# Kernel optimization log

Hardware: AMD Instinct MI355X
Metric: run time of the kernel (lower is better)

The kernel has to match this reference:

```python
import jax, jax.numpy as jnp
import numpy as np

NOISE_EPS = 1e-2


def setup_inputs() -> dict:
    key = jax.random.key(0)
    ks = jax.random.split(key, 6)
    N, D, E, H = 16384, 512, 8, 1024
    x = jax.random.normal(ks[0], (N, D), jnp.float32)
    eps = jax.random.normal(ks[1], (N, E), jnp.float32)
    w_gate = jax.random.normal(ks[2], (D, E), jnp.float32) * 0.02
    w_noise = jax.random.normal(ks[3], (D, E), jnp.float32) * 0.02
    W_h = jnp.eye(E, dtype=jnp.float32)  # module initializes W_h = eye(num_experts)
    W1 = jax.random.normal(ks[4], (E, D, H), jnp.float32) * 0.02
    b1 = jnp.zeros((E, H), jnp.float32)
    W2 = jax.random.normal(ks[5], (E, H, D), jnp.float32) * 0.02
    b2 = jnp.zeros((E, D), jnp.float32)
    return dict(x=x, eps=eps, w_gate=w_gate, w_noise=w_noise, W_h=W_h,
                W1=W1, b1=b1, W2=W2, b2=b2, k=2, capacity=5120)


def reference(x, eps, w_gate, w_noise, W_h, W1, b1, W2, b2, k, capacity):
    N, D = x.shape
    E = w_gate.shape[1]
    # --- noisy top-k gating ---
    clean_logits = (x @ w_gate) @ W_h                       # [N, E]
    noise_stddev = jax.nn.softplus(x @ w_noise) + NOISE_EPS  # [N, E]
    noisy_logits = clean_logits + eps * noise_stddev
    top_vals, top_idx = jax.lax.top_k(noisy_logits, k)       # [N, k]
    top_gates = jax.nn.softmax(top_vals, axis=-1)
    gates = jnp.zeros((N, E), x.dtype).at[jnp.arange(N)[:, None], top_idx].set(top_gates)
    # --- capacity masking: keep the first `capacity` routed tokens per expert (batch order) ---
    active = gates > 0
    rank = jnp.cumsum(active, axis=0) - 1                    # per-expert arrival rank
    keep = active & (rank < capacity)
    gates = jnp.where(keep, gates, jnp.zeros((), x.dtype))
    # --- dispatch into fixed [E, capacity] buffers (dummy slot absorbs dropped writes) ---
    flat = jnp.where(keep, jnp.arange(E)[None, :] * capacity + rank, E * capacity)  # [N, E]
    tok = jnp.broadcast_to(jnp.arange(N, dtype=jnp.int32)[:, None], (N, E))
    buf = jnp.zeros(E * capacity + 1, jnp.int32).at[flat].set(tok)[:E * capacity].reshape(E, capacity)
    gbuf = jnp.zeros(E * capacity + 1, x.dtype).at[flat].set(gates)[:E * capacity].reshape(E, capacity)
    x_exp = x[buf]                                           # [E, C, D] gather
    # --- per-expert 1-layer FFN (grouped GEMM) ---
    h = jax.nn.relu(jnp.einsum('ecd,edh->ech', x_exp, W1) + b1[:, None, :])
    y_exp = jnp.einsum('ech,eho->eco', h, W2) + b2[:, None, :]
    # --- weighted scatter-combine (unfilled slots have gate 0, so they add nothing) ---
    weighted = y_exp * gbuf[..., None]
    combined = jnp.zeros((N, D), x.dtype).at[buf.reshape(-1)].add(weighted.reshape(-1, D))
    return combined
```

## Files before the change

kernel.cpp:

```cpp
#include <hip/hip_runtime.h>
#include <hip/hip_bf16.h>
#include <cstdint>

#define NTOK 16384
#define DIM 512
#define NEXP 8
#define HID 1024
#define CAPACITY 5120

typedef __attribute__((ext_vector_type(8))) short bf16x8;
typedef __attribute__((ext_vector_type(4))) float f32x4;
typedef unsigned long long u64;

__device__ __forceinline__ unsigned short f2bf(float f) {
    unsigned u = __float_as_uint(f);
    unsigned r = (u + 0x7FFFu + ((u >> 16) & 1u)) >> 16;
    return (unsigned short)r;
}

#define GLDS16(gp, lp) __builtin_amdgcn_global_load_lds( \
    (const __attribute__((address_space(1))) void*)(gp), \
    (__attribute__((address_space(3))) void*)(lp), 16, 0, 0)

__global__ __launch_bounds__(256) void gating_kernel(
    const float* __restrict__ x, const float* __restrict__ eps,
    const float* __restrict__ wg, const float* __restrict__ wn,
    const float* __restrict__ Wh, int2* __restrict__ rec)
{
    int w = threadIdx.x >> 6, lane = threadIdx.x & 63;
    int n = blockIdx.x * 4 + w;
    float ag[8], an[8];
#pragma unroll
    for (int e = 0; e < 8; ++e) { ag[e] = 0.f; an[e] = 0.f; }
    const float* xr = x + (size_t)n * DIM;
#pragma unroll
    for (int i = 0; i < DIM / 64; ++i) {
        int d = i * 64 + lane;
        float xv = xr[d];
        const float4* g4 = reinterpret_cast<const float4*>(wg + (size_t)d * 8);
        const float4* n4 = reinterpret_cast<const float4*>(wn + (size_t)d * 8);
        float4 a0 = g4[0], a1 = g4[1], b0 = n4[0], b1v = n4[1];
        ag[0] += xv * a0.x; ag[1] += xv * a0.y; ag[2] += xv * a0.z; ag[3] += xv * a0.w;
        ag[4] += xv * a1.x; ag[5] += xv * a1.y; ag[6] += xv * a1.z; ag[7] += xv * a1.w;
        an[0] += xv * b0.x; an[1] += xv * b0.y; an[2] += xv * b0.z; an[3] += xv * b0.w;
        an[4] += xv * b1v.x; an[5] += xv * b1v.y; an[6] += xv * b1v.z; an[7] += xv * b1v.w;
    }
#pragma unroll
    for (int off = 32; off; off >>= 1) {
#pragma unroll
        for (int e = 0; e < 8; ++e) {
            ag[e] += __shfl_xor(ag[e], off);
            an[e] += __shfl_xor(an[e], off);
        }
    }
    float noisy[8];
#pragma unroll
    for (int e = 0; e < 8; ++e) {
        float c = 0.f;
#pragma unroll
        for (int j = 0; j < 8; ++j) c += ag[j] * Wh[j * 8 + e];
        float v = an[e];
        float sp = fmaxf(v, 0.f) + log1pf(expf(-fabsf(v)));
        noisy[e] = c + eps[(size_t)n * 8 + e] * (sp + 1e-2f);
    }
    int i1 = 0; float v1 = noisy[0];
#pragma unroll
    for (int e = 1; e < 8; ++e) if (noisy[e] > v1) { v1 = noisy[e]; i1 = e; }
    int i2 = -1; float v2 = -3.4e38f;
#pragma unroll
    for (int e = 0; e < 8; ++e) if (e != i1 && noisy[e] > v2) { v2 = noisy[e]; i2 = e; }
    float ex = expf(v2 - v1);
    float g1 = 1.f / (1.f + ex);
    if (lane == 0)
        rec[n] = make_int2(i1 | (i2 << 8), __float_as_int(g1));
}

__global__ __launch_bounds__(1024) void scan_local(
    const int2* __restrict__ rec, unsigned* __restrict__ lrank, int* __restrict__ btot)
{
    __shared__ u64 wtot[16];
    __shared__ int wprefix[16][8];
    int tid = threadIdx.x, w = tid >> 6, lane = tid & 63;
    int n = blockIdx.x * 1024 + tid;
    int2 r = rec[n];
    int e1 = r.x & 0xFF, e2 = (r.x >> 8) & 0xFF;
    u64 m = (1ULL << (e1 * 8)) | (1ULL << (e2 * 8));
    u64 incl = m;
#pragma unroll
    for (int off = 1; off < 64; off <<= 1) {
        u64 v = __shfl_up(incl, off);
        if (lane >= off) incl += v;
    }
    if (lane == 63) wtot[w] = incl;
    __syncthreads();
    if (tid < 128) {
        int e = tid & 7, ww = tid >> 3;
        int s = 0;
        for (int j = 0; j < ww; ++j) s += (int)((wtot[j] >> (e * 8)) & 0xFF);
        wprefix[ww][e] = s;
        if (ww == 15)
            btot[blockIdx.x * 8 + e] = s + (int)((wtot[15] >> (e * 8)) & 0xFF);
    }
    __syncthreads();
    u64 excl = incl - m;
    unsigned l1 = (unsigned)(wprefix[w][e1] + (int)((excl >> (e1 * 8)) & 0xFF));
    unsigned l2 = (unsigned)(wprefix[w][e2] + (int)((excl >> (e2 * 8)) & 0xFF));
    lrank[n] = l1 | (l2 << 16);
}

__global__ __launch_bounds__(64) void scan_offs(
    const int* __restrict__ btot, int* __restrict__ off, int* __restrict__ counts,
    const int* __restrict__ cap_p)
{
    int e = threadIdx.x;
    if (e >= 8) return;
    int cap = *cap_p; if (cap > CAPACITY) cap = CAPACITY;
    int run = 0;
    for (int b = 0; b < 16; ++b) {
        off[b * 8 + e] = run;
        run += btot[b * 8 + e];
    }
    counts[e] = min(run, cap);
}

__global__ __launch_bounds__(1024) void scatter_k(
    const int2* __restrict__ rec, const unsigned* __restrict__ lrank,
    const int* __restrict__ off, const int* __restrict__ cap_p,
    int* __restrict__ buf, float* __restrict__ gbuf)
{
    int tid = threadIdx.x, b = blockIdx.x;
    int n = b * 1024 + tid;
    int cap = *cap_p; if (cap > CAPACITY) cap = CAPACITY;
    int2 r = rec[n];
    int e1 = r.x & 0xFF, e2 = (r.x >> 8) & 0xFF;
    float g1 = __int_as_float(r.y), g2 = 1.f - g1;
    unsigned lr = lrank[n];
    int r1 = off[b * 8 + e1] + (int)(lr & 0xFFFF);
    int r2 = off[b * 8 + e2] + (int)(lr >> 16);
    if (r1 < cap) { buf[e1 * CAPACITY + r1] = n; gbuf[e1 * CAPACITY + r1] = g1; }
    if (r2 < cap) { buf[e2 * CAPACITY + r2] = n; gbuf[e2 * CAPACITY + r2] = g2; }
}

__global__ __launch_bounds__(256) void cvt_x(const float* __restrict__ in,
                                             unsigned short* __restrict__ out, int n)
{
    int i = (blockIdx.x * 256 + threadIdx.x) * 8;
    if (i >= n) return;
    float4 a = *reinterpret_cast<const float4*>(in + i);
    float4 b = *reinterpret_cast<const float4*>(in + i + 4);
    int4 v;
    v.x = f2bf(a.x) | ((int)f2bf(a.y) << 16);
    v.y = f2bf(a.z) | ((int)f2bf(a.w) << 16);
    v.z = f2bf(b.x) | ((int)f2bf(b.y) << 16);
    v.w = f2bf(b.z) | ((int)f2bf(b.w) << 16);
    *reinterpret_cast<int4*>(out + i) = v;
}

__global__ __launch_bounds__(256) void tcvt(const float* __restrict__ in,
                                            unsigned short* __restrict__ out, int R, int C)
{
    __shared__ float tile[32][33];
    int z = blockIdx.z;
    int c0 = blockIdx.x * 32, r0 = blockIdx.y * 32;
    int tx = threadIdx.x, ty = threadIdx.y;
    const float* inz = in + (size_t)z * R * C;
    unsigned short* outz = out + (size_t)z * R * C;
#pragma unroll
    for (int j = 0; j < 32; j += 8)
        tile[ty + j][tx] = inz[(size_t)(r0 + ty + j) * C + c0 + tx];
    __syncthreads();
#pragma unroll
    for (int j = 0; j < 32; j += 8)
        outz[(size_t)(c0 + ty + j) * R + r0 + tx] = f2bf(tile[tx][ty + j]);
}

template <int MODE>
__global__ __launch_bounds__(256, 4) void ffn_gemm(
    const unsigned short* __restrict__ A, const unsigned short* __restrict__ Bt,
    const float* __restrict__ bias, unsigned short* __restrict__ Hout,
    float* __restrict__ Out, const int* __restrict__ buf,
    const float* __restrict__ gbuf, const int* __restrict__ counts,
    int Ka, int Nd)
{
    int flat = blockIdx.x + gridDim.x * (blockIdx.y + gridDim.y * blockIdx.z);
    int e  = flat & 7;
    int rr = flat >> 3;
    int tn = rr % gridDim.y;
    int tmb = rr / gridDim.y;

    int cnt = counts[e];
    if (tmb * 256 >= cnt) return;
    int tid = threadIdx.x, w = tid >> 6, lane = tid & 63;
    int q = lane >> 4, rl = lane & 15;
    int ebase = e * CAPACITY;
    int wm = w >> 1, wn = w & 1;

    __shared__ __align__(16) char lds[32768];
    char* As = lds;
    char* Bs = lds + 16384;

    unsigned boff[4];
    int srow[4], skp[4];
#pragma unroll
    for (int i = 0; i < 4; ++i) {
        int p = (w * 4 + i) * 64 + lane;
        int row = p >> 3, kp = p & 7;
        int c = kp ^ (row & 7);
        srow[i] = row; skp[i] = c;
        boff[i] = (unsigned)(e * Nd + tn * 128 + row) * Ka + c * 8;
    }

    for (int it = 0; it < 2; ++it) {
        int tm = tmb * 2 + it;
        if (tm * 128 >= cnt) break;

        unsigned aoff[4];
#pragma unroll
        for (int i = 0; i < 4; ++i) {
            int slot = tm * 128 + srow[i];
            if (MODE == 1) {
                int tok = (slot < cnt) ? buf[ebase + slot] : 0;
                aoff[i] = (unsigned)tok * Ka + skp[i] * 8;
            } else {
                aoff[i] = (unsigned)(ebase + slot) * Ka + skp[i] * 8;
            }
        }

        f32x4 acc[4][4];
#pragma unroll
        for (int mi = 0; mi < 4; ++mi)
#pragma unroll
            for (int ni = 0; ni < 4; ++ni)
                acc[mi][ni] = (f32x4){0.f, 0.f, 0.f, 0.f};

        for (int k0 = 0; k0 < Ka; k0 += 64) {
#pragma unroll
            for (int i = 0; i < 4; ++i) {
                GLDS16(A + aoff[i] + k0, As + (w * 4 + i) * 1024);
                GLDS16(Bt + boff[i] + k0, Bs + (w * 4 + i) * 1024);
            }
            __syncthreads();
#pragma unroll
            for (int kk = 0; kk < 2; ++kk) {
                bf16x8 af[4], bfr[4];
#pragma unroll
                for (int mi = 0; mi < 4; ++mi) {
                    int row = wm * 64 + mi * 16 + rl;
                    int cc = (kk * 4 + q) ^ (row & 7);
                    af[mi] = *reinterpret_cast<const bf16x8*>(As + row * 128 + cc * 16);
                }
#pragma unroll
                for (int ni = 0; ni < 4; ++ni) {
                    int row = wn * 64 + ni * 16 + rl;
                    int cc = (kk * 4 + q) ^ (row & 7);
                    bfr[ni] = *reinterpret_cast<const bf16x8*>(Bs + row * 128 + cc * 16);
                }
#pragma unroll
                for (int mi = 0; mi < 4; ++mi)
#pragma unroll
                    for (int ni = 0; ni < 4; ++ni)
                        acc[mi][ni] = __builtin_amdgcn_mfma_f32_16x16x32_bf16(
                            af[mi], bfr[ni], acc[mi][ni], 0, 0, 0);
            }
            __syncthreads();
        }

        if (MODE == 1) {
#pragma unroll
            for (int ni = 0; ni < 4; ++ni) {
                int gcol = tn * 128 + wn * 64 + ni * 16 + rl;
                float bv = bias[e * Nd + gcol];
#pragma unroll
                for (int mi = 0; mi < 4; ++mi) {
#pragma unroll
                    for (int r = 0; r < 4; ++r) {
                        int grow = tm * 128 + wm * 64 + mi * 16 + q * 4 + r;
                        float v = fmaxf(acc[mi][ni][r] + bv, 0.f);
                        Hout[(size_t)(ebase + grow) * HID + gcol] = f2bf(v);
                    }
                }
            }
        } else {
#pragma unroll
            for (int ni = 0; ni < 4; ++ni) {
                int gcol = tn * 128 + wn * 64 + ni * 16 + rl;
                float bv = bias[e * Nd + gcol];
#pragma unroll
                for (int mi = 0; mi < 4; ++mi) {
#pragma unroll
                    for (int r = 0; r < 4; ++r) {
                        int grow = tm * 128 + wm * 64 + mi * 16 + q * 4 + r;
                        if (grow < cnt) {
                            int tok = buf[ebase + grow];
                            float g = gbuf[ebase + grow];
                            float v = (acc[mi][ni][r] + bv) * g;
                            atomicAdd(Out + (size_t)tok * DIM + gcol, v);
                        }
                    }
                }
            }
        }
    }
}

extern "C" void kernel_launch(void* const* d_in, const int* in_sizes, int n_in,
                              void* d_out, int out_size, void* d_ws, size_t ws_size,
                              hipStream_t stream)
{
    const float* x   = (const float*)d_in[0];
    const float* eps = (const float*)d_in[1];
    const float* wg  = (const float*)d_in[2];
    const float* wn  = (const float*)d_in[3];
    const float* Wh  = (const float*)d_in[4];
    const float* W1  = (const float*)d_in[5];
    const float* b1  = (const float*)d_in[6];
    const float* W2  = (const float*)d_in[7];
    const float* b2  = (const float*)d_in[8];
    const int* capp  = (const int*)d_in[10];

    char* ws = (char*)d_ws;
    unsigned short* xg   = (unsigned short*)(ws);
    unsigned short* w1t  = (unsigned short*)(ws + 41943040);
    unsigned short* w2t  = (unsigned short*)(ws + 50331648);
    unsigned short* hK   = (unsigned short*)(ws + 58720256);
    int*      buf    = (int*)     (ws + 142606336);
    float*    gbuf   = (float*)   (ws + 142770176);
    int2*     rec    = (int2*)    (ws + 142934016);
    unsigned* lrank  = (unsigned*)(ws + 143065088);
    int*      btot   = (int*)     (ws + 143130624);
    int*      off    = (int*)     (ws + 143131136);
    int*      counts = (int*)     (ws + 143131648);

    float* out = (float*)d_out;
    hipMemsetAsync(out, 0, (size_t)out_size * sizeof(float), stream);

    gating_kernel<<<NTOK / 4, 256, 0, stream>>>(x, eps, wg, wn, Wh, rec);
    scan_local<<<16, 1024, 0, stream>>>(rec, lrank, btot);
    scan_offs<<<1, 64, 0, stream>>>(btot, off, counts, capp);
    scatter_k<<<16, 1024, 0, stream>>>(rec, lrank, off, capp, buf, gbuf);
    cvt_x<<<NTOK * DIM / 8 / 256, 256, 0, stream>>>(x, xg, NTOK * DIM);
    tcvt<<<dim3(HID / 32, DIM / 32, NEXP), dim3(32, 8), 0, stream>>>(W1, w1t, DIM, HID);
    tcvt<<<dim3(DIM / 32, HID / 32, NEXP), dim3(32, 8), 0, stream>>>(W2, w2t, HID, DIM);

    ffn_gemm<1><<<dim3(CAPACITY / 256, HID / 128, NEXP), 256, 0, stream>>>(
        xg, w1t, b1, hK, nullptr, buf, gbuf, counts, DIM, HID);
    ffn_gemm<0><<<dim3(CAPACITY / 256, DIM / 128, NEXP), 256, 0, stream>>>(
        hK, w2t, b2, nullptr, out, buf, gbuf, counts, HID, DIM);
}
```

Before: 221.3 us.

## Triple-buffer GEMM k-loop with async LDS loads and explicit vmcnt waits

Replaces the single-buffered 64-wide k-step loop in the expert FFN GEMM with a three-stage ring of 32-wide k tiles in LDS. Loads for tile t+2 are issued before computing on tile t, and partial s_waitcnt vmcnt counts are used so global-to-LDS traffic overlaps MFMA work. The LDS swizzle changes to match 64-byte rows. LDS use rises to 48KB and occupancy is lowered to 3 blocks per CU. The hand-written waitcnt/barrier sequencing is fragile and depends on the compiler not adding other outstanding vector memory ops.

```diff
diff --git a/kernel.cpp b/kernel.cpp
--- a/kernel.cpp
+++ b/kernel.cpp
@@ -174,8 +174,19 @@
         outz[(size_t)(c0 + ty + j) * R + r0 + tx] = f2bf(tile[tx][ty + j]);
 }
 
+
+#define STAGE32(T, BI)                                           \
+  {                                                              \
+    int k0_ = (T) * 32;                                          \
+    char* d_ = lds + (BI) * 16384 + w * 2048;                    \
+    GLDS16(A + aoff[0] + k0_, d_);                               \
+    GLDS16(A + aoff[1] + k0_, d_ + 1024);                        \
+    GLDS16(Bt + boff[0] + k0_, d_ + 8192);                       \
+    GLDS16(Bt + boff[1] + k0_, d_ + 9216);                       \
+  }
+
 template <int MODE>
-__global__ __launch_bounds__(256, 4) void ffn_gemm(
+__global__ __launch_bounds__(256, 3) void ffn_gemm(
     const unsigned short* __restrict__ A, const unsigned short* __restrict__ Bt,
     const float* __restrict__ bias, unsigned short* __restrict__ Hout,
     float* __restrict__ Out, const int* __restrict__ buf,
@@ -195,34 +206,37 @@
     int ebase = e * CAPACITY;
     int wm = w >> 1, wn = w & 1;
 
-    __shared__ __align__(16) char lds[32768];
-    char* As = lds;
-    char* Bs = lds + 16384;
-
-    unsigned boff[4];
-    int srow[4], skp[4];
-#pragma unroll
-    for (int i = 0; i < 4; ++i) {
-        int p = (w * 4 + i) * 64 + lane;
-        int row = p >> 3, kp = p & 7;
-        int c = kp ^ (row & 7);
-        srow[i] = row; skp[i] = c;
-        boff[i] = (unsigned)(e * Nd + tn * 128 + row) * Ka + c * 8;
-    }
+    __shared__ __align__(16) char lds[49152];
+
+    int srow[2], skc[2];
+#pragma unroll
+    for (int i = 0; i < 2; ++i) {
+        int p = (w * 2 + i) * 64 + lane;
+        int row = p >> 2, kp = p & 3;
+        srow[i] = row;
+        skc[i] = kp ^ ((row >> 1) & 3);
+    }
+    unsigned boff[2];
+#pragma unroll
+    for (int i = 0; i < 2; ++i)
+        boff[i] = (unsigned)(e * Nd + tn * 128 + srow[i]) * Ka + skc[i] * 8;
+
+    int ccb = (q ^ ((rl >> 1) & 3)) << 4;
+    int nt = Ka >> 5;
 
     for (int it = 0; it < 2; ++it) {
         int tm = tmb * 2 + it;
         if (tm * 128 >= cnt) break;
 
-        unsigned aoff[4];
-#pragma unroll
-        for (int i = 0; i < 4; ++i) {
+        unsigned aoff[2];
+#pragma unroll
+        for (int i = 0; i < 2; ++i) {
             int slot = tm * 128 + srow[i];
             if (MODE == 1) {
                 int tok = (slot < cnt) ? buf[ebase + slot] : 0;
-                aoff[i] = (unsigned)tok * Ka + skp[i] * 8;
+                aoff[i] = (unsigned)tok * Ka + skc[i] * 8;
             } else {
-                aoff[i] = (unsigned)(ebase + slot) * Ka + skp[i] * 8;
+                aoff[i] = (unsigned)(ebase + slot) * Ka + skc[i] * 8;
             }
         }
 
@@ -233,36 +247,44 @@
             for (int ni = 0; ni < 4; ++ni)
                 acc[mi][ni] = (f32x4){0.f, 0.f, 0.f, 0.f};
 
-        for (int k0 = 0; k0 < Ka; k0 += 64) {
-#pragma unroll
-            for (int i = 0; i < 4; ++i) {
-                GLDS16(A + aoff[i] + k0, As + (w * 4 + i) * 1024);
-                GLDS16(Bt + boff[i] + k0, Bs + (w * 4 + i) * 1024);
-            }
-            __syncthreads();
-#pragma unroll
-            for (int kk = 0; kk < 2; ++kk) {
-                bf16x8 af[4], bfr[4];
-#pragma unroll
-                for (int mi = 0; mi < 4; ++mi) {
-                    int row = wm * 64 + mi * 16 + rl;
-                    int cc = (kk * 4 + q) ^ (row & 7);
-                    af[mi] = *reinterpret_cast<const bf16x8*>(As + row * 128 + cc * 16);
-                }
-#pragma unroll
-                for (int ni = 0; ni < 4; ++ni) {
-                    int row = wn * 64 + ni * 16 + rl;
-                    int cc = (kk * 4 + q) ^ (row & 7);
-                    bfr[ni] = *reinterpret_cast<const bf16x8*>(Bs + row * 128 + cc * 16);
-                }
-#pragma unroll
-                for (int mi = 0; mi < 4; ++mi)
-#pragma unroll
-                    for (int ni = 0; ni < 4; ++ni)
-                        acc[mi][ni] = __builtin_amdgcn_mfma_f32_16x16x32_bf16(
-                            af[mi], bfr[ni], acc[mi][ni], 0, 0, 0);
-            }
-            __syncthreads();
+        STAGE32(0, 0);
+        STAGE32(1, 1);
+
+        int bcur = 0, bst = 2;
+        for (int t = 0; t < nt; ++t) {
+            if (t + 2 < nt) {
+                STAGE32(t + 2, bst);
+                bst = (bst == 2) ? 0 : bst + 1;
+                asm volatile("s_waitcnt vmcnt(8)" ::: "memory");
+            } else if (t + 2 == nt) {
+                asm volatile("s_waitcnt vmcnt(4)" ::: "memory");
+            } else {
+                asm volatile("s_waitcnt vmcnt(0)" ::: "memory");
+            }
+            asm volatile("s_barrier" ::: "memory");
+
+            const char* As = lds + bcur * 16384;
+            const char* Bs = As + 8192;
+            bf16x8 af[4], bfr[4];
+#pragma unroll
+            for (int mi = 0; mi < 4; ++mi) {
+                int row = wm * 64 + mi * 16 + rl;
+                af[mi] = *reinterpret_cast<const bf16x8*>(As + row * 64 + ccb);
+            }
+#pragma unroll
+            for (int ni = 0; ni < 4; ++ni) {
+                int row = wn * 64 + ni * 16 + rl;
+                bfr[ni] = *reinterpret_cast<const bf16x8*>(Bs + row * 64 + ccb);
+            }
+#pragma unroll
+            for (int mi = 0; mi < 4; ++mi)
+#pragma unroll
+                for (int ni = 0; ni < 4; ++ni)
+                    acc[mi][ni] = __builtin_amdgcn_mfma_f32_16x16x32_bf16(
+                        af[mi], bfr[ni], acc[mi][ni], 0, 0, 0);
+
+            asm volatile("s_barrier" ::: "memory");
+            bcur = (bcur == 2) ? 0 : bcur + 1;
         }
 
         if (MODE == 1) {
```

Result: no change. 223.9 us (+1.2%).

## Compute both 128-row M tiles together to reuse B tile across 256 rows

Applied to the files above, without the earlier changes.

The grouped FFN GEMM used to process two 128-row M tiles one after the other, reloading the B (weight) tile for each. It now loads both A tiles and one B tile per k-step into a larger 48KB LDS buffer and keeps two accumulator sets, so each B fragment feeds twice as many MFMAs. This halves B traffic and barriers per output. In exchange it doubles accumulator registers and drops launch bounds to 2 blocks per CU, which lowers occupancy, and it computes the second tile even when it lies beyond the expert's token count.

```diff
diff --git a/kernel.cpp b/kernel.cpp
--- a/kernel.cpp
+++ b/kernel.cpp
@@ -175,7 +175,7 @@
 }
 
 template <int MODE>
-__global__ __launch_bounds__(256, 4) void ffn_gemm(
+__global__ __launch_bounds__(256, 2) void ffn_gemm(
     const unsigned short* __restrict__ A, const unsigned short* __restrict__ Bt,
     const float* __restrict__ bias, unsigned short* __restrict__ Hout,
     float* __restrict__ Out, const int* __restrict__ buf,
@@ -195,107 +195,112 @@
     int ebase = e * CAPACITY;
     int wm = w >> 1, wn = w & 1;
 
-    __shared__ __align__(16) char lds[32768];
-    char* As = lds;
-    char* Bs = lds + 16384;
-
-    unsigned boff[4];
-    int srow[4], skp[4];
+    __shared__ __align__(16) char lds[49152];
+
+    unsigned a0off[4], a1off[4], boff[4];
 #pragma unroll
     for (int i = 0; i < 4; ++i) {
         int p = (w * 4 + i) * 64 + lane;
         int row = p >> 3, kp = p & 7;
         int c = kp ^ (row & 7);
-        srow[i] = row; skp[i] = c;
+        int s0 = tmb * 256 + row, s1 = s0 + 128;
+        if (MODE == 1) {
+            int t0 = (s0 < cnt) ? buf[ebase + s0] : 0;
+            int t1 = (s1 < cnt) ? buf[ebase + s1] : 0;
+            a0off[i] = (unsigned)t0 * Ka + c * 8;
+            a1off[i] = (unsigned)t1 * Ka + c * 8;
+        } else {
+            a0off[i] = (unsigned)(ebase + s0) * Ka + c * 8;
+            a1off[i] = (unsigned)(ebase + s1) * Ka + c * 8;
+        }
         boff[i] = (unsigned)(e * Nd + tn * 128 + row) * Ka + c * 8;
     }
 
-    for (int it = 0; it < 2; ++it) {
-        int tm = tmb * 2 + it;
-        if (tm * 128 >= cnt) break;
-
-        unsigned aoff[4];
+    f32x4 acc0[4][4], acc1[4][4];
+#pragma unroll
+    for (int mi = 0; mi < 4; ++mi)
+#pragma unroll
+        for (int ni = 0; ni < 4; ++ni) {
+            acc0[mi][ni] = (f32x4){0.f, 0.f, 0.f, 0.f};
+            acc1[mi][ni] = (f32x4){0.f, 0.f, 0.f, 0.f};
+        }
+
+    for (int k0 = 0; k0 < Ka; k0 += 64) {
 #pragma unroll
         for (int i = 0; i < 4; ++i) {
-            int slot = tm * 128 + srow[i];
-            if (MODE == 1) {
-                int tok = (slot < cnt) ? buf[ebase + slot] : 0;
-                aoff[i] = (unsigned)tok * Ka + skp[i] * 8;
-            } else {
-                aoff[i] = (unsigned)(ebase + slot) * Ka + skp[i] * 8;
+            GLDS16(A + a0off[i] + k0, lds + (w * 4 + i) * 1024);
+            GLDS16(A + a1off[i] + k0, lds + 16384 + (w * 4 + i) * 1024);
+            GLDS16(Bt + boff[i] + k0, lds + 32768 + (w * 4 + i) * 1024);
+        }
+        __syncthreads();
+#pragma unroll
+        for (int kk = 0; kk < 2; ++kk) {
+            bf16x8 af0[4], af1[4], bfr[4];
+#pragma unroll
+            for (int mi = 0; mi < 4; ++mi) {
+                int row = wm * 64 + mi * 16 + rl;
+                int cc = (kk * 4 + q) ^ (row & 7);
+                af0[mi] = *reinterpret_cast<const bf16x8*>(lds + row * 128 + cc * 16);
+                af1[mi] = *reinterpret_cast<const bf16x8*>(lds + 16384 + row * 128 + cc * 16);
             }
-        }
-
-        f32x4 acc[4][4];
-#pragma unroll
-        for (int mi = 0; mi < 4; ++mi)
-#pragma unroll
-            for (int ni = 0; ni < 4; ++ni)
-                acc[mi][ni] = (f32x4){0.f, 0.f, 0.f, 0.f};
-
-        for (int k0 = 0; k0 < Ka; k0 += 64) {
-#pragma unroll
-            for (int i = 0; i < 4; ++i) {
-                GLDS16(A + aoff[i] + k0, As + (w * 4 + i) * 1024);
-                GLDS16(Bt + boff[i] + k0, Bs + (w * 4 + i) * 1024);
+#pragma unroll
+            for (int ni = 0; ni < 4; ++ni) {
+                int row = wn * 64 + ni * 16 + rl;
+                int cc = (kk * 4 + q) ^ (row & 7);
+                bfr[ni] = *reinterpret_cast<const bf16x8*>(lds + 32768 + row * 128 + cc * 16);
             }
-            __syncthreads();
-#pragma unroll
-            for (int kk = 0; kk < 2; ++kk) {
-                bf16x8 af[4], bfr[4];
-#pragma unroll
-                for (int mi = 0; mi < 4; ++mi) {
-                    int row = wm * 64 + mi * 16 + rl;
-                    int cc = (kk * 4 + q) ^ (row & 7);
-                    af[mi] = *reinterpret_cast<const bf16x8*>(As + row * 128 + cc * 16);
+#pragma unroll
+            for (int mi = 0; mi < 4; ++mi)
+#pragma unroll
+                for (int ni = 0; ni < 4; ++ni) {
+                    acc0[mi][ni] = __builtin_amdgcn_mfma_f32_16x16x32_bf16(
+                        af0[mi], bfr[ni], acc0[mi][ni], 0, 0, 0);
+                    acc1[mi][ni] = __builtin_amdgcn_mfma_f32_16x16x32_bf16(
+                        af1[mi], bfr[ni], acc1[mi][ni], 0, 0, 0);
                 }
-#pragma unroll
-                for (int ni = 0; ni < 4; ++ni) {
-                    int row = wn * 64 + ni * 16 + rl;
-                    int cc = (kk * 4 + q) ^ (row & 7);
-                    bfr[ni] = *reinterpret_cast<const bf16x8*>(Bs + row * 128 + cc * 16);
-                }
-#pragma unroll
-                for (int mi = 0; mi < 4; ++mi)
-#pragma unroll
-                    for (int ni = 0; ni < 4; ++ni)
-                        acc[mi][ni] = __builtin_amdgcn_mfma_f32_16x16x32_bf16(
-                            af[mi], bfr[ni], acc[mi][ni], 0, 0, 0);
-            }
-            __syncthreads();
-        }
-
-        if (MODE == 1) {
-#pragma unroll
-            for (int ni = 0; ni < 4; ++ni) {
-                int gcol = tn * 128 + wn * 64 + ni * 16 + rl;
-                float bv = bias[e * Nd + gcol];
-#pragma unroll
-                for (int mi = 0; mi < 4; ++mi) {
-#pragma unroll
-                    for (int r = 0; r < 4; ++r) {
-                        int grow = tm * 128 + wm * 64 + mi * 16 + q * 4 + r;
-                        float v = fmaxf(acc[mi][ni][r] + bv, 0.f);
-                        Hout[(size_t)(ebase + grow) * HID + gcol] = f2bf(v);
-                    }
+        }
+        __syncthreads();
+    }
+
+    if (MODE == 1) {
+#pragma unroll
+        for (int ni = 0; ni < 4; ++ni) {
+            int gcol = tn * 128 + wn * 64 + ni * 16 + rl;
+            float bv = bias[e * Nd + gcol];
+#pragma unroll
+            for (int mi = 0; mi < 4; ++mi) {
+#pragma unroll
+                for (int r = 0; r < 4; ++r) {
+                    int g0 = tmb * 256 + wm * 64 + mi * 16 + q * 4 + r;
+                    float v0 = fmaxf(acc0[mi][ni][r] + bv, 0.f);
+                    Hout[(size_t)(ebase + g0) * HID + gcol] = f2bf(v0);
+                    float v1 = fmaxf(acc1[mi][ni][r] + bv, 0.f);
+                    Hout[(size_t)(ebase + g0 + 128) * HID + gcol] = f2bf(v1);
                 }
             }
-        } else {
-#pragma unroll
-            for (int ni = 0; ni < 4; ++ni) {
-                int gcol = tn * 128 + wn * 64 + ni * 16 + rl;
-                float bv = bias[e * Nd + gcol];
-#pragma unroll
-                for (int mi = 0; mi < 4; ++mi) {
-#pragma unroll
-                    for (int r = 0; r < 4; ++r) {
-                        int grow = tm * 128 + wm * 64 + mi * 16 + q * 4 + r;
-                        if (grow < cnt) {
-                            int tok = buf[ebase + grow];
-                            float g = gbuf[ebase + grow];
-                            float v = (acc[mi][ni][r] + bv) * g;
-                            atomicAdd(Out + (size_t)tok * DIM + gcol, v);
-                        }
+        }
+    } else {
+#pragma unroll
+        for (int ni = 0; ni < 4; ++ni) {
+            int gcol = tn * 128 + wn * 64 + ni * 16 + rl;
+            float bv = bias[e * Nd + gcol];
+#pragma unroll
+            for (int mi = 0; mi < 4; ++mi) {
+#pragma unroll
+                for (int r = 0; r < 4; ++r) {
+                    int g0 = tmb * 256 + wm * 64 + mi * 16 + q * 4 + r;
+                    if (g0 < cnt) {
+                        int tok = buf[ebase + g0];
+                        float g = gbuf[ebase + g0];
+                        atomicAdd(Out + (size_t)tok * DIM + gcol,
+                                  (acc0[mi][ni][r] + bv) * g);
+                    }
+                    int g1r = g0 + 128;
+                    if (g1r < cnt) {
+                        int tok = buf[ebase + g1r];
+                        float g = gbuf[ebase + g1r];
+                        atomicAdd(Out + (size_t)tok * DIM + gcol,
+                                  (acc1[mi][ni][r] + bv) * g);
                     }
                 }
             }
```

Measured after the change: 260.7 us. +17.8%, slower.
